# Kernel tuning notes

Hardware: AMD Instinct MI355X
Metric: run time of the kernel (lower is better)

The kernel has to match this reference:

```python
import jax, jax.numpy as jnp
import numpy as np

INPUT_DIM = 512
OUTPUT_DIM = 512
DEGREE = 8
BATCH = 16384


def setup_inputs() -> dict:
    key = jax.random.key(0)
    kx, kc = jax.random.split(key)
    x = jax.random.normal(kx, (BATCH, INPUT_DIM), dtype=jnp.float32)
    cheby_coeffs = jax.random.normal(kc, (INPUT_DIM, OUTPUT_DIM, DEGREE + 1), dtype=jnp.float32) / jnp.sqrt(
        jnp.float32(INPUT_DIM * (DEGREE + 1))
    )
    return {"x": x, "cheby_coeffs": cheby_coeffs}


def reference(x, cheby_coeffs):
    degree = cheby_coeffs.shape[-1] - 1
    arange = jnp.arange(degree + 1, dtype=x.dtype)  # [d]
    t = jnp.tanh(x)  # [b, i], squash into [-1, 1]
    theta = jnp.arccos(t)[..., None] * arange  # [b, i, d]
    basis = jnp.cos(theta)  # Chebyshev T_n(tanh(x)) = cos(n * arccos(tanh(x)))
    y = jnp.einsum('bid,iod->bo', basis, cheby_coeffs)
    return y
```

## Files before the change

### kernel.cpp

```cpp
#include <hip/hip_runtime.h>
#include <hip/hip_bf16.h>
#include <stdint.h>


#define BM 128
#define BN 128
#define BK 64
#define NSTEPS 64
#define IN_DIM 512
#define OUT_DIM 512

typedef __attribute__((ext_vector_type(8))) short short8;
typedef __attribute__((ext_vector_type(8))) unsigned short ushort8;
typedef __attribute__((ext_vector_type(4))) float f32x4;

__device__ __forceinline__ unsigned short f2bf(float f) {
  __hip_bfloat16 h = __float2bfloat16(f);
  return __builtin_bit_cast(unsigned short, h);
}

__device__ __forceinline__ float fast_tanh(float v) {
  float e = __expf(v + v);
  return 1.0f - 2.0f * __builtin_amdgcn_rcpf(e + 1.0f);
}

__device__ __forceinline__ void gload_lds16(const void* g, void* l) {
  __builtin_amdgcn_global_load_lds(
      (const __attribute__((address_space(1))) unsigned int*)(uintptr_t)g,
      (__attribute__((address_space(3))) unsigned int*)(uintptr_t)l,
      16, 0, 0);
}

__global__ __launch_bounds__(256) void cheby_reorder_b(
    const float* __restrict__ coeffs, unsigned char* __restrict__ bws) {
  const int g = blockIdx.x * 256 + threadIdx.x;
  const int i = g & 511;
  const int o = g >> 9;
  const int nb = o >> 7, nl = o & 127;
  const int itile = i >> 5, il = i & 31;
  const float* cp = coeffs + (size_t)i * 4608 + (size_t)o * 9;
  const int swz = (nl & 7) << 4;
#pragma unroll
  for (int p = 0; p < 4; ++p) {
    const size_t base =
        ((size_t)(nb * 64 + itile * 4 + p) << 14) + (size_t)nl * 128;
    *(unsigned short*)(bws + base + ((il * 2) ^ swz)) = f2bf(cp[1 + 2 * p]);
    *(unsigned short*)(bws + base + ((64 + il * 2) ^ swz)) =
        f2bf(cp[2 + 2 * p]);
  }
}

__global__ __launch_bounds__(64) void cheby_colsum(
    const float* __restrict__ coeffs, float* __restrict__ cs) {
  const int o = blockIdx.x;
  const int l = threadIdx.x;
  float s = 0.0f;
#pragma unroll
  for (int j = 0; j < 8; ++j)
    s += coeffs[(size_t)(l + j * 64) * 4608 + (size_t)o * 9];
#pragma unroll
  for (int off = 32; off > 0; off >>= 1) s += __shfl_down(s, off, 64);
  if (l == 0) cs[o] = s;
}

__global__ __launch_bounds__(256, 3) void cheby_gemm(
    const float* __restrict__ x, const unsigned char* __restrict__ bws,
    const float* __restrict__ colsum, float* __restrict__ out) {
  const int bid = blockIdx.x;
  const int m0 = (bid >> 2) * BM;
  const int nblk = bid & 3;
  const int n0 = nblk * BN;
  const int tid = threadIdx.x;
  const int lane = tid & 63;
  const int wid = tid >> 6;
  const int wm = (wid >> 1) * 64;
  const int wn = (wid & 1) * 64;
  const int l15 = lane & 15;
  const int lhi = lane >> 4;

  __shared__ __align__(16) unsigned char As[BM * 128];
  __shared__ __align__(16) unsigned char Bs[BN * 128];

  const int srow = tid >> 1;
  const int ihalf = tid & 1;
  unsigned char* Arow = As + srow * 128;
  const int aswz = (srow & 7) << 4;
  const int wbase = ihalf * 32;

  float t2[16], Tm1[16], Tm2[16];
  f32x4 acc[4][4];
#pragma unroll
  for (int a = 0; a < 4; ++a)
#pragma unroll
    for (int b = 0; b < 4; ++b) acc[a][b] = (f32x4){0.f, 0.f, 0.f, 0.f};

  const unsigned char* bchunk0 = bws + ((size_t)(nblk * 64) << 14);

  for (int s = 0; s < NSTEPS; ++s) {
    const unsigned char* gsrc =
        bchunk0 + ((size_t)s << 14) + wid * 4096 + lane * 16;
    unsigned char* ldst = Bs + wid * 4096;
    gload_lds16(gsrc, ldst);
    gload_lds16(gsrc + 1024, ldst + 1024);
    gload_lds16(gsrc + 2048, ldst + 2048);
    gload_lds16(gsrc + 3072, ldst + 3072);

    const int p = s & 3;
    if (p == 0) {
      const int itile = s >> 2;
      const float* xp =
          x + (size_t)(m0 + srow) * IN_DIM + itile * 32 + ihalf * 16;
#pragma unroll
      for (int j = 0; j < 4; ++j) {
        const float4 v = reinterpret_cast<const float4*>(xp)[j];
        const float a0 = fast_tanh(v.x);
        const float a1 = fast_tanh(v.y);
        const float a2 = fast_tanh(v.z);
        const float a3 = fast_tanh(v.w);
        Tm2[4 * j + 0] = a0; Tm2[4 * j + 1] = a1;
        Tm2[4 * j + 2] = a2; Tm2[4 * j + 3] = a3;
        t2[4 * j + 0] = a0 + a0; t2[4 * j + 1] = a1 + a1;
        t2[4 * j + 2] = a2 + a2; t2[4 * j + 3] = a3 + a3;
        Tm1[4 * j + 0] = __builtin_fmaf(a0 + a0, a0, -1.0f);
        Tm1[4 * j + 1] = __builtin_fmaf(a1 + a1, a1, -1.0f);
        Tm1[4 * j + 2] = __builtin_fmaf(a2 + a2, a2, -1.0f);
        Tm1[4 * j + 3] = __builtin_fmaf(a3 + a3, a3, -1.0f);
      }
    } else {
#pragma unroll
      for (int e = 0; e < 16; ++e) {
        const float Ta = __builtin_fmaf(t2[e], Tm1[e], -Tm2[e]);
        const float Tb = __builtin_fmaf(t2[e], Ta, -Tm1[e]);
        Tm2[e] = Ta;
        Tm1[e] = Tb;
      }
    }
    ushort8 pa0, pa1, pb0, pb1;
#pragma unroll
    for (int j = 0; j < 8; ++j) {
      pa0[j] = f2bf(Tm2[j]);
      pa1[j] = f2bf(Tm2[j + 8]);
      pb0[j] = f2bf(Tm1[j]);
      pb1[j] = f2bf(Tm1[j + 8]);
    }
    *(ushort8*)(Arow + ((wbase) ^ aswz)) = pa0;
    *(ushort8*)(Arow + ((wbase + 16) ^ aswz)) = pa1;
    *(ushort8*)(Arow + ((64 + wbase) ^ aswz)) = pb0;
    *(ushort8*)(Arow + ((64 + wbase + 16) ^ aswz)) = pb1;

    __syncthreads();

#pragma unroll
    for (int ks = 0; ks < 2; ++ks) {
      short8 af[4];
#pragma unroll
      for (int fm = 0; fm < 4; ++fm) {
        const int row = wm + fm * 16 + l15;
        af[fm] = *(const short8*)(
            As + row * 128 + ((ks * 64 + lhi * 16) ^ ((row & 7) << 4)));
      }
#pragma unroll
      for (int fn = 0; fn < 4; ++fn) {
        const int row = wn + fn * 16 + l15;
        const short8 bf = *(const short8*)(
            Bs + row * 128 + ((ks * 64 + lhi * 16) ^ ((row & 7) << 4)));
#pragma unroll
        for (int fm = 0; fm < 4; ++fm)
          acc[fm][fn] = __builtin_amdgcn_mfma_f32_16x16x32_bf16(
              af[fm], bf, acc[fm][fn], 0, 0, 0);
      }
    }
    __syncthreads();
  }

  float csv[4];
#pragma unroll
  for (int fn = 0; fn < 4; ++fn) csv[fn] = colsum[n0 + wn + fn * 16 + l15];
#pragma unroll
  for (int fm = 0; fm < 4; ++fm) {
    const int r0 = m0 + wm + fm * 16 + lhi * 4;
#pragma unroll
    for (int fn = 0; fn < 4; ++fn) {
      const int col = n0 + wn + fn * 16 + l15;
#pragma unroll
      for (int r = 0; r < 4; ++r)
        out[(size_t)(r0 + r) * OUT_DIM + col] = acc[fm][fn][r] + csv[fn];
    }
  }
}

extern "C" void kernel_launch(void* const* d_in, const int* in_sizes, int n_in,
                              void* d_out, int out_size, void* d_ws,
                              size_t ws_size, hipStream_t stream) {
  const float* x = (const float*)d_in[0];
  const float* coeffs = (const float*)d_in[1];
  float* out = (float*)d_out;
  unsigned char* bws = (unsigned char*)d_ws;
  float* cs = (float*)((unsigned char*)d_ws + ((size_t)4 << 20));

  hipLaunchKernelGGL(cheby_reorder_b, dim3(1024), dim3(256), 0, stream, coeffs,
                     bws);
  hipLaunchKernelGGL(cheby_colsum, dim3(512), dim3(64), 0, stream, coeffs, cs);
  hipLaunchKernelGGL(cheby_gemm, dim3(512), dim3(256), 0, stream, x, bws, cs,
                     out);
}
```

Before: 97.53 us.

## Double-buffer B tile in LDS and prefetch next K-step asynchronously

Result: slower. 100.7 us (+3.2%).

```diff
diff --git a/kernel.cpp b/kernel.cpp
--- a/kernel.cpp
+++ b/kernel.cpp
@@ -79,7 +79,7 @@
   const int lhi = lane >> 4;
 
   __shared__ __align__(16) unsigned char As[BM * 128];
-  __shared__ __align__(16) unsigned char Bs[BN * 128];
+  __shared__ __align__(16) unsigned char Bs[2][BN * 128];
 
   const int srow = tid >> 1;
   const int ihalf = tid & 1;
@@ -95,18 +95,32 @@
     for (int b = 0; b < 4; ++b) acc[a][b] = (f32x4){0.f, 0.f, 0.f, 0.f};
 
   const unsigned char* bchunk0 = bws + ((size_t)(nblk * 64) << 14);
-
-  for (int s = 0; s < NSTEPS; ++s) {
-    const unsigned char* gsrc =
-        bchunk0 + ((size_t)s << 14) + wid * 4096 + lane * 16;
-    unsigned char* ldst = Bs + wid * 4096;
+  const int goff = wid * 4096 + lane * 16;
+
+  {
+    const unsigned char* gsrc = bchunk0 + goff;
+    unsigned char* ldst = &Bs[0][0] + wid * 4096;
     gload_lds16(gsrc, ldst);
     gload_lds16(gsrc + 1024, ldst + 1024);
     gload_lds16(gsrc + 2048, ldst + 2048);
     gload_lds16(gsrc + 3072, ldst + 3072);
-
-    const int p = s & 3;
-    if (p == 0) {
+  }
+
+  for (int s = 0; s < NSTEPS; ++s) {
+    const int p = s & 1;
+
+    {
+      const int snext = (s < NSTEPS - 1) ? s + 1 : NSTEPS - 1;
+      const unsigned char* gsrc = bchunk0 + ((size_t)snext << 14) + goff;
+      unsigned char* ldst = &Bs[p ^ 1][0] + wid * 4096;
+      gload_lds16(gsrc, ldst);
+      gload_lds16(gsrc + 1024, ldst + 1024);
+      gload_lds16(gsrc + 2048, ldst + 2048);
+      gload_lds16(gsrc + 3072, ldst + 3072);
+    }
+
+    const int q = s & 3;
+    if (q == 0) {
       const int itile = s >> 2;
       const float* xp =
           x + (size_t)(m0 + srow) * IN_DIM + itile * 32 + ihalf * 16;
@@ -148,8 +162,10 @@
     *(ushort8*)(Arow + ((64 + wbase) ^ aswz)) = pb0;
     *(ushort8*)(Arow + ((64 + wbase + 16) ^ aswz)) = pb1;
 
-    __syncthreads();
-
+    asm volatile("s_waitcnt vmcnt(4) lgkmcnt(0)" ::: "memory");
+    __builtin_amdgcn_s_barrier();
+
+    const unsigned char* Bcur = &Bs[p][0];
 #pragma unroll
     for (int ks = 0; ks < 2; ++ks) {
       short8 af[4];
@@ -163,14 +179,15 @@
       for (int fn = 0; fn < 4; ++fn) {
         const int row = wn + fn * 16 + l15;
         const short8 bf = *(const short8*)(
-            Bs + row * 128 + ((ks * 64 + lhi * 16) ^ ((row & 7) << 4)));
+            Bcur + row * 128 + ((ks * 64 + lhi * 16) ^ ((row & 7) << 4)));
 #pragma unroll
         for (int fm = 0; fm < 4; ++fm)
           acc[fm][fn] = __builtin_amdgcn_mfma_f32_16x16x32_bf16(
               af[fm], bf, acc[fm][fn], 0, 0, 0);
       }
     }
-    __syncthreads();
+
+    __builtin_amdgcn_s_barrier();
   }
 
   float csv[4];
```
